# Optimization experiments

Hardware: AMD Instinct MI355X
Metric: run time of the kernel (lower is better)

Reference implementation:

```python
import jax, jax.numpy as jnp
import numpy as np

N_HEAD = 16

def setup_inputs() -> dict:
    key = jax.random.key(0)
    k1, k2, k3 = jax.random.split(key, 3)
    B, T, C = 4, 2048, 1024
    x = jax.random.normal(k1, (B, T, C), dtype=jnp.float32)
    Wqkv = jax.random.normal(k2, (C, 3 * C), dtype=jnp.float32) * (C ** -0.5)
    bqkv = jnp.zeros((3 * C,), dtype=jnp.float32)
    Wout = jax.random.normal(k3, (C, C), dtype=jnp.float32) * (C ** -0.5)
    bout = jnp.zeros((C,), dtype=jnp.float32)
    return {"x": x, "Wqkv": Wqkv, "bqkv": bqkv, "Wout": Wout, "bout": bout}

def reference(x, Wqkv, bqkv, Wout, bout):
    B, T, C = x.shape
    H = N_HEAD
    hd = C // H
    scale = hd ** -0.5
    qkv = x @ Wqkv + bqkv                      # [B,T,3C]
    q, k, v = jnp.split(qkv, 3, axis=-1)
    # [B,T,C] -> [B,H,T,hd]
    q = q.reshape(B, T, H, hd).transpose(0, 2, 1, 3)
    k = k.reshape(B, T, H, hd).transpose(0, 2, 1, 3)
    v = v.reshape(B, T, H, hd).transpose(0, 2, 1, 3)
    attn = jnp.einsum('bhqd,bhkd->bhqk', q, k) * scale  # [B,H,T,T]
    mask = jnp.tril(jnp.ones((T, T), dtype=bool))
    attn = jnp.where(mask[None, None], attn, -jnp.inf)
    attn = jax.nn.softmax(attn, axis=-1)       # dropout p=0.0 -> identity
    out = jnp.einsum('bhqk,bhkd->bhqd', attn, v)
    out = out.transpose(0, 2, 1, 3).reshape(B, T, C)
    out = out @ Wout + bout
    return (out, k, v)
```

## Files before the change

kernel.cpp:

```cpp
#include <hip/hip_runtime.h>
#include <stdint.h>

typedef short bf16x8 __attribute__((ext_vector_type(8)));
typedef float f32x4 __attribute__((ext_vector_type(4)));

#define MFMA16(A, B, C) __builtin_amdgcn_mfma_f32_16x16x32_bf16((A), (B), (C), 0, 0, 0)

__device__ inline unsigned short f2bf(float x) {
    unsigned int b = __builtin_bit_cast(unsigned int, x);
    b += 0x7fffu + ((b >> 16) & 1u);
    return (unsigned short)(b >> 16);
}
__device__ inline unsigned pack2bf(float x, float y) {
    unsigned a = __builtin_bit_cast(unsigned, x) + 0x8000u;
    unsigned b = __builtin_bit_cast(unsigned, y) + 0x8000u;
    return __builtin_amdgcn_perm(b, a, 0x07060302u);
}

#if __has_builtin(__builtin_amdgcn_exp2f)
#define EXP2(x) __builtin_amdgcn_exp2f(x)
#else
__device__ inline float fast_exp2_(float x) {
    float r;
    asm("v_exp_f32 %0, %1" : "=v"(r) : "v"(x));
    return r;
}
#define EXP2(x) fast_exp2_(x)
#endif

typedef __attribute__((address_space(1))) const void glob_cv;
typedef __attribute__((address_space(3))) void lds_v;
__device__ __forceinline__ void async_copy16(void* lds, const void* g) {
    __builtin_amdgcn_global_load_lds((glob_cv*)g, (lds_v*)lds, 16, 0, 0);
}

__global__ __launch_bounds__(256) void prep_kernel(
    const float* __restrict__ x, unsigned short* __restrict__ xb,
    const float* __restrict__ Wqkv, unsigned short* __restrict__ WqkvT,
    const float* __restrict__ Wout, unsigned short* __restrict__ WoutT) {
    int bid = blockIdx.x;
    if (bid < 4096) {
        size_t g = (size_t)bid * 256 + threadIdx.x;
        float4 a = ((const float4*)x)[g * 2 + 0];
        float4 b = ((const float4*)x)[g * 2 + 1];
        union { unsigned short u[8]; uint4 v; } r;
        r.u[0] = f2bf(a.x); r.u[1] = f2bf(a.y); r.u[2] = f2bf(a.z); r.u[3] = f2bf(a.w);
        r.u[4] = f2bf(b.x); r.u[5] = f2bf(b.y); r.u[6] = f2bf(b.z); r.u[7] = f2bf(b.w);
        ((uint4*)xb)[g] = r.v;
        return;
    }
    const float* in;
    unsigned short* out;
    int R, C, bx, by;
    if (bid < 4096 + 3072) {
        in = Wqkv; out = WqkvT; R = 1024; C = 3072;
        int idx = bid - 4096;
        bx = idx % 96; by = idx / 96;
    } else {
        in = Wout; out = WoutT; R = 1024; C = 1024;
        int idx = bid - 7168;
        bx = idx % 32; by = idx / 32;
    }
    __shared__ float tile[32][33];
    int tx = threadIdx.x & 31, ty = threadIdx.x >> 5;
    int c0 = bx * 32, r0 = by * 32;
#pragma unroll
    for (int i = 0; i < 4; i++)
        tile[ty + i * 8][tx] = in[(size_t)(r0 + ty + i * 8) * C + c0 + tx];
    __syncthreads();
#pragma unroll
    for (int i = 0; i < 4; i++)
        out[(size_t)(c0 + ty + i * 8) * R + r0 + tx] = f2bf(tile[tx][ty + i * 8]);
}

template <int MODE>
__global__ __launch_bounds__(256, 4) void gemm_bt_kernel(
    const unsigned short* __restrict__ A, const unsigned short* __restrict__ Bt,
    const float* __restrict__ bias, int K,
    unsigned short* __restrict__ q_out, float* __restrict__ k_out, float* __restrict__ v_out,
    unsigned short* __restrict__ vT, float* __restrict__ c_out) {
    __shared__ __align__(16) unsigned short As[2 * 128 * 32];
    __shared__ __align__(16) unsigned short Bs[2 * 128 * 32];
    int tid = threadIdx.x;
    int w = tid >> 6, l = tid & 63;
    int quad = l >> 4, cl = l & 15;
    int wm = w & 1, wn = w >> 1;
    int m0 = blockIdx.y * 128, n0 = blockIdx.x * 128;

    f32x4 acc[4][4] = {};

    int srow = w * 16 + (l >> 2);
    int scol = ((l & 3) ^ ((l >> 2) & 3)) * 8;
    const unsigned short* Ap = A + (size_t)(m0 + srow) * K + scol;
    const unsigned short* Bp = Bt + (size_t)(n0 + srow) * K + scol;
    const size_t rstep = (size_t)64 * K;
    const int pk = (quad ^ (cl & 3)) * 8;

#define STAGE(bo_, kk_)                                              \
    do {                                                             \
        unsigned short* a0 = &As[(bo_) * 4096 + w * 512];            \
        unsigned short* b0 = &Bs[(bo_) * 4096 + w * 512];            \
        async_copy16(a0, Ap + (kk_));                                \
        async_copy16(a0 + 2048, Ap + rstep + (kk_));                 \
        async_copy16(b0, Bp + (kk_));                                \
        async_copy16(b0 + 2048, Bp + rstep + (kk_));                 \
    } while (0)

#define CSTEP(bo_)                                                                            \
    do {                                                                                      \
        bf16x8 af[4], bfr[4];                                                                 \
        _Pragma("unroll")                                                                     \
        for (int t = 0; t < 4; t++) {                                                         \
            af[t]  = *(const bf16x8*)&As[(bo_) * 4096 + (wm * 64 + t * 16 + cl) * 32 + pk];   \
            bfr[t] = *(const bf16x8*)&Bs[(bo_) * 4096 + (wn * 64 + t * 16 + cl) * 32 + pk];   \
        }                                                                                     \
        _Pragma("unroll")                                                                     \
        for (int mt = 0; mt < 4; mt++)                                                        \
            _Pragma("unroll")                                                                 \
            for (int nt = 0; nt < 4; nt++)                                                    \
                acc[mt][nt] = MFMA16(af[mt], bfr[nt], acc[mt][nt]);                           \
    } while (0)

    STAGE(0, 0);

    for (int k0 = 0; k0 < K; k0 += 64) {
        __syncthreads();
        if (k0 + 32 < K) STAGE(1, k0 + 32);
        CSTEP(0);
        __syncthreads();
        if (k0 + 64 < K) STAGE(0, k0 + 64);
        CSTEP(1);
    }
#undef CSTEP
#undef STAGE

    if (MODE == 0) {
#pragma unroll
        for (int mt = 0; mt < 4; mt++)
#pragma unroll
            for (int nt = 0; nt < 4; nt++) {
                int n = n0 + wn * 64 + nt * 16 + cl;
                float bn = bias[n];
                int sec = n >> 10, cc = n & 1023, h = cc >> 6, d = cc & 63;
                int mb = m0 + wm * 64 + mt * 16 + quad * 4;
                int b = mb >> 11, t = mb & 2047;
                size_t idx0 = ((size_t)(b * 16 + h) * 2048 + t) * 64 + d;
                if (sec == 0) {
#pragma unroll
                    for (int r = 0; r < 4; r++)
                        q_out[idx0 + (size_t)r * 64] = f2bf((acc[mt][nt][r] + bn) * 0.18033688011112042f);
                } else if (sec == 1) {
#pragma unroll
                    for (int r = 0; r < 4; r++)
                        k_out[idx0 + (size_t)r * 64] = acc[mt][nt][r] + bn;
                } else {
#pragma unroll
                    for (int r = 0; r < 4; r++)
                        v_out[idx0 + (size_t)r * 64] = acc[mt][nt][r] + bn;
                    uint2 vv;
                    vv.x = pack2bf(acc[mt][nt][0] + bn, acc[mt][nt][1] + bn);
                    vv.y = pack2bf(acc[mt][nt][2] + bn, acc[mt][nt][3] + bn);
                    *(uint2*)&vT[((size_t)(b * 16 + h) * 64 + d) * 2048 + t] = vv;
                }
            }
    } else {
#pragma unroll
        for (int mt = 0; mt < 4; mt++)
#pragma unroll
            for (int nt = 0; nt < 4; nt++) {
                int n = n0 + wn * 64 + nt * 16 + cl;
                float bn = bias[n];
#pragma unroll
                for (int r = 0; r < 4; r++) {
                    int m = m0 + wm * 64 + mt * 16 + quad * 4 + r;
                    c_out[(size_t)m * 1024 + n] = acc[mt][nt][r] + bn;
                }
            }
    }
}

__global__ __launch_bounds__(256) void attn_kernel(
    const unsigned short* __restrict__ Q,
    const float* __restrict__ Kin,
    const unsigned short* __restrict__ Vt,
    unsigned short* __restrict__ Out) {
    __shared__ __align__(16) unsigned short Ks[2 * 64 * 72];
    __shared__ __align__(16) unsigned short Vts[2 * 64 * 64];
    __shared__ __align__(16) unsigned short Ps[128 * 72];
    int tid = threadIdx.x;
    int w = tid >> 6, l = tid & 63;
    int quad = l >> 4, cl = l & 15;
    int cl7 = cl & 7;
    int bh = blockIdx.x;
    int b = bh >> 4, h = bh & 15;
    int qt = 15 - (int)blockIdx.y;
    int qw0 = qt * 128 + w * 32;
    int nkt = 2 * qt + 2;

    int srow = tid >> 2, sch = tid & 3;
    const float* kbase = Kin + ((size_t)bh * 2048 + srow) * 64 + sch * 16;
    unsigned lK = srow * 72 + sch * 16;
    int vrow = 8 * w + (l >> 3);
    int vchk = (l & 7) ^ (l >> 3);
    const unsigned short* vg = Vt + ((size_t)bh * 64 + vrow) * 2048 + vchk * 8;

    const unsigned short* qb = Q + ((size_t)bh * 2048 + qw0 + cl) * 64;
    bf16x8 qf[2][2];
    qf[0][0] = *(const bf16x8*)(qb + quad * 8);
    qf[0][1] = *(const bf16x8*)(qb + 32 + quad * 8);
    qf[1][0] = *(const bf16x8*)(qb + 16 * 64 + quad * 8);
    qf[1][1] = *(const bf16x8*)(qb + 16 * 64 + 32 + quad * 8);

    f32x4 accO[2][4] = {};
    float lloc[2] = {0.f, 0.f};

    float4 kr0, kr1, kr2, kr3;
    {
        const float4* kpp = (const float4*)kbase;
        kr0 = kpp[0]; kr1 = kpp[1]; kr2 = kpp[2]; kr3 = kpp[3];
    }
    {
        unsigned short* vsb = &Vts[w * 512];
        async_copy16(vsb, vg);
        async_copy16(vsb + 2048, vg + (size_t)32 * 2048);
    }

    for (int kt = 0; kt < nkt; ++kt) {
        unsigned bo = (unsigned)(kt & 1);
        uint4 c0, c1;
        c0.x = pack2bf(kr0.x, kr0.y); c0.y = pack2bf(kr0.z, kr0.w);
        c0.z = pack2bf(kr1.x, kr1.y); c0.w = pack2bf(kr1.z, kr1.w);
        c1.x = pack2bf(kr2.x, kr2.y); c1.y = pack2bf(kr2.z, kr2.w);
        c1.z = pack2bf(kr3.x, kr3.y); c1.w = pack2bf(kr3.z, kr3.w);
        *(uint4*)&Ks[bo * 4608 + lK] = c0;
        *(uint4*)&Ks[bo * 4608 + lK + 8] = c1;
        __syncthreads();

        if (kt + 1 < nkt) {
            const float4* kpp = (const float4*)(kbase + (size_t)(kt + 1) * 4096);
            kr0 = kpp[0]; kr1 = kpp[1]; kr2 = kpp[2]; kr3 = kpp[3];
            unsigned short* vsb = &Vts[(bo ^ 1) * 4096 + w * 512];
            async_copy16(vsb, vg + (size_t)(kt + 1) * 64);
            async_copy16(vsb + 2048, vg + (size_t)32 * 2048 + (size_t)(kt + 1) * 64);
        }
        if (kt * 64 > qw0 + 31) continue;

        f32x4 s[2][4];
        __builtin_amdgcn_s_setprio(1);
#pragma unroll
        for (int mt = 0; mt < 4; mt++) {
            bf16x8 kf0 = *(const bf16x8*)&Ks[bo * 4608 + (mt * 16 + cl) * 72 + quad * 8];
            bf16x8 kf1 = *(const bf16x8*)&Ks[bo * 4608 + (mt * 16 + cl) * 72 + 32 + quad * 8];
#pragma unroll
            for (int ng = 0; ng < 2; ng++) {
                f32x4 a = {};
                a = MFMA16(kf0, qf[ng][0], a);
                a = MFMA16(kf1, qf[ng][1], a);
                s[ng][mt] = a;
            }
        }
        __builtin_amdgcn_s_setprio(0);
        if (kt * 64 + 63 > qw0) {
#pragma unroll
            for (int ng = 0; ng < 2; ng++) {
                int qg = qw0 + ng * 16 + cl;
#pragma unroll
                for (int mt = 0; mt < 4; mt++)
#pragma unroll
                    for (int r = 0; r < 4; r++) {
                        int kv = kt * 64 + mt * 16 + quad * 4 + r;
                        if (kv > qg) s[ng][mt][r] = -1e30f;
                    }
            }
        }
        bf16x8 pf[2][2];
#pragma unroll
        for (int ng = 0; ng < 2; ng++) {
            unsigned pbase = (unsigned)(w * 32 + ng * 16 + cl) * 72;
#pragma unroll
            for (int mt = 0; mt < 4; mt++) {
                float e0 = EXP2(s[ng][mt][0]);
                float e1 = EXP2(s[ng][mt][1]);
                float e2 = EXP2(s[ng][mt][2]);
                float e3 = EXP2(s[ng][mt][3]);
                lloc[ng] += (e0 + e1) + (e2 + e3);
                uint2 pv;
                pv.x = pack2bf(e0, e1);
                pv.y = pack2bf(e2, e3);
                *(uint2*)&Ps[pbase + mt * 16 + quad * 4] = pv;
            }
            pf[ng][0] = *(const bf16x8*)&Ps[pbase + quad * 8];
            pf[ng][1] = *(const bf16x8*)&Ps[pbase + 32 + quad * 8];
        }
        __builtin_amdgcn_s_setprio(1);
#pragma unroll
        for (int mt = 0; mt < 4; mt++) {
            int vr = mt * 16 + cl;
            bf16x8 vf0 = *(const bf16x8*)&Vts[bo * 4096 + vr * 64 + (quad ^ cl7) * 8];
            bf16x8 vf1 = *(const bf16x8*)&Vts[bo * 4096 + vr * 64 + ((quad | 4) ^ cl7) * 8];
#pragma unroll
            for (int ng = 0; ng < 2; ng++) {
                accO[ng][mt] = MFMA16(vf0, pf[ng][0], accO[ng][mt]);
                accO[ng][mt] = MFMA16(vf1, pf[ng][1], accO[ng][mt]);
            }
        }
        __builtin_amdgcn_s_setprio(0);
    }

#pragma unroll
    for (int ng = 0; ng < 2; ng++) {
        float lv = lloc[ng];
        lv += __shfl_xor(lv, 16);
        lv += __shfl_xor(lv, 32);
        float inv = 1.0f / lv;
        size_t obase = ((size_t)(b * 2048 + qw0 + ng * 16 + cl)) * 1024 + h * 64;
#pragma unroll
        for (int mt = 0; mt < 4; mt++) {
            uint2 ov;
            ov.x = (unsigned)f2bf(accO[ng][mt][0] * inv) | ((unsigned)f2bf(accO[ng][mt][1] * inv) << 16);
            ov.y = (unsigned)f2bf(accO[ng][mt][2] * inv) | ((unsigned)f2bf(accO[ng][mt][3] * inv) << 16);
            *(uint2*)&Out[obase + mt * 16 + quad * 4] = ov;
        }
    }
}

extern "C" void kernel_launch(void* const* d_in, const int* in_sizes, int n_in,
                              void* d_out, int out_size, void* d_ws, size_t ws_size,
                              hipStream_t stream) {
    const float* x    = (const float*)d_in[0];
    const float* Wqkv = (const float*)d_in[1];
    const float* bqkv = (const float*)d_in[2];
    const float* Wout = (const float*)d_in[3];
    const float* bout = (const float*)d_in[4];

    float* out   = (float*)d_out;
    float* k_out = out + 8388608;
    float* v_out = out + 16777216;

    char* ws = (char*)d_ws;
    unsigned short* xb    = (unsigned short*)(ws);
    unsigned short* WqkvT = (unsigned short*)(ws + 16777216);
    unsigned short* WoutT = (unsigned short*)(ws + 23068672);
    unsigned short* q_ws  = (unsigned short*)(ws + 25165824);
    unsigned short* vT    = (unsigned short*)(ws + 41943040);
    unsigned short* attn  = xb;

    prep_kernel<<<8192, 256, 0, stream>>>(x, xb, Wqkv, WqkvT, Wout, WoutT);
    gemm_bt_kernel<0><<<dim3(24, 64), 256, 0, stream>>>(xb, WqkvT, bqkv, 1024,
                                                        q_ws, k_out, v_out, vT, nullptr);
    attn_kernel<<<dim3(64, 16), 256, 0, stream>>>(q_ws, k_out, vT, attn);
    gemm_bt_kernel<1><<<dim3(8, 64), 256, 0, stream>>>(attn, WoutT, bout, 1024,
                                                       nullptr, nullptr, nullptr, nullptr, out);
}
```

Before: 294.3 us.

## Triple-buffer GEMM LDS stages with partial vmcnt waits and one barrier per step

The bf16 GEMM's K loop moves from a double-buffered pipeline with two full __syncthreads per iteration to a three-stage LDS ring. Each step waits only until the older async copies have landed (vmcnt(4)), then issues a single barrier, so the next tile's global loads overlap two compute steps instead of one. The LDS swizzle pattern also changes to a different XOR over row bits, meant to reduce bank conflicts. The extra LDS stage lowers the launch-bounds occupancy target from 4 to 3 blocks, and the unrolled tail assumes K is 64 more than a multiple of 96, which holds for K=1024.

```diff
diff --git a/kernel.cpp b/kernel.cpp
--- a/kernel.cpp
+++ b/kernel.cpp
@@ -74,13 +74,13 @@
 }
 
 template <int MODE>
-__global__ __launch_bounds__(256, 4) void gemm_bt_kernel(
+__global__ __launch_bounds__(256, 3) void gemm_bt_kernel(
     const unsigned short* __restrict__ A, const unsigned short* __restrict__ Bt,
     const float* __restrict__ bias, int K,
     unsigned short* __restrict__ q_out, float* __restrict__ k_out, float* __restrict__ v_out,
     unsigned short* __restrict__ vT, float* __restrict__ c_out) {
-    __shared__ __align__(16) unsigned short As[2 * 128 * 32];
-    __shared__ __align__(16) unsigned short Bs[2 * 128 * 32];
+    __shared__ __align__(16) unsigned short As[3 * 4096];
+    __shared__ __align__(16) unsigned short Bs[3 * 4096];
     int tid = threadIdx.x;
     int w = tid >> 6, l = tid & 63;
     int quad = l >> 4, cl = l & 15;
@@ -90,29 +90,29 @@
     f32x4 acc[4][4] = {};
 
     int srow = w * 16 + (l >> 2);
-    int scol = ((l & 3) ^ ((l >> 2) & 3)) * 8;
+    int scol = ((l & 3) ^ ((l >> 3) & 3)) * 8;
     const unsigned short* Ap = A + (size_t)(m0 + srow) * K + scol;
     const unsigned short* Bp = Bt + (size_t)(n0 + srow) * K + scol;
     const size_t rstep = (size_t)64 * K;
-    const int pk = (quad ^ (cl & 3)) * 8;
-
-#define STAGE(bo_, kk_)                                              \
+    const int pk = (quad ^ ((cl >> 1) & 3)) * 8;
+
+#define STAGE(bi_, kk_)                                              \
     do {                                                             \
-        unsigned short* a0 = &As[(bo_) * 4096 + w * 512];            \
-        unsigned short* b0 = &Bs[(bo_) * 4096 + w * 512];            \
+        unsigned short* a0 = &As[(bi_) * 4096 + w * 512];            \
+        unsigned short* b0 = &Bs[(bi_) * 4096 + w * 512];            \
         async_copy16(a0, Ap + (kk_));                                \
         async_copy16(a0 + 2048, Ap + rstep + (kk_));                 \
         async_copy16(b0, Bp + (kk_));                                \
         async_copy16(b0 + 2048, Bp + rstep + (kk_));                 \
     } while (0)
 
-#define CSTEP(bo_)                                                                            \
+#define CSTEP(bi_)                                                                            \
     do {                                                                                      \
         bf16x8 af[4], bfr[4];                                                                 \
         _Pragma("unroll")                                                                     \
         for (int t = 0; t < 4; t++) {                                                         \
-            af[t]  = *(const bf16x8*)&As[(bo_) * 4096 + (wm * 64 + t * 16 + cl) * 32 + pk];   \
-            bfr[t] = *(const bf16x8*)&Bs[(bo_) * 4096 + (wn * 64 + t * 16 + cl) * 32 + pk];   \
+            af[t]  = *(const bf16x8*)&As[(bi_) * 4096 + (wm * 64 + t * 16 + cl) * 32 + pk];   \
+            bfr[t] = *(const bf16x8*)&Bs[(bi_) * 4096 + (wn * 64 + t * 16 + cl) * 32 + pk];   \
         }                                                                                     \
         _Pragma("unroll")                                                                     \
         for (int mt = 0; mt < 4; mt++)                                                        \
@@ -121,16 +121,27 @@
                 acc[mt][nt] = MFMA16(af[mt], bfr[nt], acc[mt][nt]);                           \
     } while (0)
 
+#define KSTEP(bi_, nbi_, nk_, LAST_)                                                          \
+    do {                                                                                      \
+        if (LAST_) asm volatile("s_waitcnt vmcnt(0) lgkmcnt(0)" ::: "memory");                \
+        else       asm volatile("s_waitcnt vmcnt(4) lgkmcnt(0)" ::: "memory");                \
+        __builtin_amdgcn_s_barrier();                                                         \
+        if ((nk_) < K) STAGE(nbi_, nk_);                                                      \
+        CSTEP(bi_);                                                                           \
+    } while (0)
+
     STAGE(0, 0);
-
-    for (int k0 = 0; k0 < K; k0 += 64) {
-        __syncthreads();
-        if (k0 + 32 < K) STAGE(1, k0 + 32);
-        CSTEP(0);
-        __syncthreads();
-        if (k0 + 64 < K) STAGE(0, k0 + 64);
-        CSTEP(1);
-    }
+    STAGE(1, 32);
+
+    int k0 = 0;
+    for (; k0 + 96 <= K; k0 += 96) {
+        KSTEP(0, 2, k0 + 64, 0);
+        KSTEP(1, 0, k0 + 96, 0);
+        KSTEP(2, 1, k0 + 128, 0);
+    }
+    KSTEP(0, 2, K, 0);
+    KSTEP(1, 0, K, 1);
+#undef KSTEP
 #undef CSTEP
 #undef STAGE
 
```

After: 293.8 us (median of 2 runs). About the same (-0.2%).
